# Kernel tuning notes

Measured on AMD Instinct MI355X. Metric: run time of the kernel, lower is better.

## Reference

```python
import jax, jax.numpy as jnp
import numpy as np

N_NODES = 50000
N_EDGES = 800000
D_IN = 256
DIM_H = 256
N_GRAPHS = 500
N_OUT = 10
BN_EPS = 1e-5


def _mlp(h, W1, b1, gamma, beta, mean, var, W2, b2):
    # Linear -> BatchNorm1d (eval, running stats) -> ReLU -> Linear -> ReLU
    h = h @ W1 + b1
    h = (h - mean) * (gamma / jnp.sqrt(var + BN_EPS)) + beta
    h = jax.nn.relu(h)
    return jax.nn.relu(h @ W2 + b2)


def _gin_conv(x, src, dst, params):
    # PyG GINConv with eps=0: out = nn(x + sum_{j in N(i)} x_j)
    agg = jax.ops.segment_sum(x[src], dst, num_segments=N_NODES)
    return _mlp(x + agg, *params)


def setup_inputs() -> dict:
    key = jax.random.key(0)
    ks = jax.random.split(key, 24)
    x = jax.random.normal(ks[0], (N_NODES, D_IN), dtype=jnp.float32)
    edge_index = jax.random.randint(ks[1], (2, N_EDGES), 0, N_NODES, dtype=jnp.int64)
    batch = jnp.sort(jax.random.randint(ks[2], (N_NODES,), 0, N_GRAPHS, dtype=jnp.int64))

    def lin(k, fan_in, fan_out):
        s = 1.0 / np.sqrt(fan_in)
        kw, kb = jax.random.split(k)
        W = jax.random.uniform(kw, (fan_in, fan_out), minval=-s, maxval=s, dtype=jnp.float32)
        b = jax.random.uniform(kb, (fan_out,), minval=-s, maxval=s, dtype=jnp.float32)
        return W, b

    def bn(k, d):
        k1, k2, k3, k4 = jax.random.split(k, 4)
        gamma = 1.0 + 0.1 * jax.random.normal(k1, (d,), dtype=jnp.float32)
        beta = 0.1 * jax.random.normal(k2, (d,), dtype=jnp.float32)
        mean = 0.1 * jax.random.normal(k3, (d,), dtype=jnp.float32)
        var = jax.random.uniform(k4, (d,), minval=0.5, maxval=1.5, dtype=jnp.float32)
        return gamma, beta, mean, var

    W1a, b1a = lin(ks[3], D_IN, DIM_H)
    g1a, be1a, m1a, v1a = bn(ks[4], DIM_H)
    W2a, b2a = lin(ks[5], DIM_H, DIM_H)
    W1b, b1b = lin(ks[6], DIM_H, DIM_H)
    g1b, be1b, m1b, v1b = bn(ks[7], DIM_H)
    W2b, b2b = lin(ks[8], DIM_H, DIM_H)
    lin1_W, lin1_b = lin(ks[9], DIM_H * 2, DIM_H * 3)
    lin2_W, lin2_b = lin(ks[10], DIM_H * 3, N_OUT)

    return dict(x=x, edge_index=edge_index, batch=batch,
                W1a=W1a, b1a=b1a, g1a=g1a, be1a=be1a, m1a=m1a, v1a=v1a, W2a=W2a, b2a=b2a,
                W1b=W1b, b1b=b1b, g1b=g1b, be1b=be1b, m1b=m1b, v1b=v1b, W2b=W2b, b2b=b2b,
                lin1_W=lin1_W, lin1_b=lin1_b, lin2_W=lin2_W, lin2_b=lin2_b)


def reference(x, edge_index, batch,
              W1a, b1a, g1a, be1a, m1a, v1a, W2a, b2a,
              W1b, b1b, g1b, be1b, m1b, v1b, W2b, b2b,
              lin1_W, lin1_b, lin2_W, lin2_b):
    src, dst = edge_index[0], edge_index[1]
    h1 = _gin_conv(x, src, dst, (W1a, b1a, g1a, be1a, m1a, v1a, W2a, b2a))
    h2 = _gin_conv(h1, src, dst, (W1b, b1b, g1b, be1b, m1b, v1b, W2b, b2b))
    p1 = jax.ops.segment_sum(h1, batch, num_segments=N_GRAPHS)  # global_add_pool
    p2 = jax.ops.segment_sum(h2, batch, num_segments=N_GRAPHS)
    h = jnp.concatenate([p1, p2], axis=1)
    h = jax.nn.relu(h @ lin1_W + lin1_b)
    # dropout p=0.6 is identity in eval mode
    h = h @ lin2_W + lin2_b
    return jax.nn.log_softmax(h, axis=1)
```

## Files before the change

### kernel.cpp

```cpp
#include <hip/hip_runtime.h>

#define N_NODES 50000
#define MPAD 50176
#define N_EDGES 800000
#define DIM 256
#define N_GRAPHS 500
#define N_OUT 10
#define BN_EPS 1e-5f
#define SCAN_BS 1024
#define KSPLIT 4
#define SORT_CAP 96

typedef unsigned int u32;
typedef short bf16x8 __attribute__((ext_vector_type(8)));
typedef unsigned short us8 __attribute__((ext_vector_type(8)));
typedef float f32x4 __attribute__((ext_vector_type(4)));

typedef __attribute__((address_space(1))) const unsigned int gas_u32;
typedef __attribute__((address_space(3))) unsigned int las_u32;

__device__ inline void g2l16(const void* g, void* l) {
    __builtin_amdgcn_global_load_lds((gas_u32*)g, (las_u32*)l, 16, 0, 0);
}

__device__ inline float b2f(unsigned short u) {
    union { u32 i; float f; } c; c.i = ((u32)u) << 16; return c.f;
}
__device__ inline unsigned short f2b(float f) {
    u32 x = __builtin_bit_cast(u32, f);
    return (unsigned short)((x + 0x7FFFu + ((x >> 16) & 1u)) >> 16);
}

__device__ inline int mid_addr(int row, int col) {
    return row * 512 + ((((col >> 3) ^ (row & 31)) << 4) | ((col & 7) << 1));
}

__global__ void zero_i(int* __restrict__ p, int n) {
    int i = blockIdx.x * blockDim.x + threadIdx.x;
    if (i < n) p[i] = 0;
}
__global__ void hist_dst(const int* __restrict__ dst, int* __restrict__ deg) {
    int e = blockIdx.x * blockDim.x + threadIdx.x;
    if (e < N_EDGES) atomicAdd(&deg[dst[e]], 1);
}
__global__ void scan_phase1(const int* __restrict__ deg, int* __restrict__ rowptr,
                            int* __restrict__ bsum, int n) {
    __shared__ int sh[SCAN_BS];
    int i = blockIdx.x * SCAN_BS + threadIdx.x;
    int v = (i < n) ? deg[i] : 0;
    sh[threadIdx.x] = v;
    __syncthreads();
    for (int off = 1; off < SCAN_BS; off <<= 1) {
        int t = (threadIdx.x >= off) ? sh[threadIdx.x - off] : 0;
        __syncthreads();
        sh[threadIdx.x] += t;
        __syncthreads();
    }
    if (i < n) rowptr[i] = sh[threadIdx.x] - v;
    if (threadIdx.x == SCAN_BS - 1) bsum[blockIdx.x] = sh[threadIdx.x];
}
__global__ void scan_phase2(int* __restrict__ bsum, int nb) {
    if (threadIdx.x == 0 && blockIdx.x == 0) {
        int run = 0;
        for (int b = 0; b < nb; b++) { int v = bsum[b]; bsum[b] = run; run += v; }
    }
}
__global__ void scan_phase3(int* __restrict__ rowptr, int* __restrict__ cursor,
                            const int* __restrict__ bsum, int n) {
    int i = blockIdx.x * SCAN_BS + threadIdx.x;
    if (i < n) {
        int v = rowptr[i] + bsum[blockIdx.x];
        rowptr[i] = v;
        cursor[i] = v;
    }
    if (i == 0) rowptr[n] = N_EDGES;
}
__global__ void fill_csr(const int* __restrict__ src, const int* __restrict__ dst,
                         int* __restrict__ cursor, int* __restrict__ col) {
    int e = blockIdx.x * blockDim.x + threadIdx.x;
    if (e < N_EDGES) {
        int p = atomicAdd(&cursor[dst[e]], 1);
        col[p] = src[e];
    }
}
__global__ void sort_csr(const int* __restrict__ rowptr, int* __restrict__ col) {
    __shared__ int buf[4][SORT_CAP];
    int node = blockIdx.x * 4 + (threadIdx.x >> 6);
    if (node >= N_NODES) return;
    int lane = threadIdx.x & 63;
    int w = threadIdx.x >> 6;
    int s = rowptr[node], e = rowptr[node + 1];
    int L = e - s;
    if (L <= 1 || L > SORT_CAP) return;
    for (int i = lane; i < L; i += 64) buf[w][i] = col[s + i];
    asm volatile("s_waitcnt lgkmcnt(0) vmcnt(0)" ::: "memory");
    for (int pass = 0; pass < L; pass++) {
        int base = 2 * lane + (pass & 1);
        if (base + 1 < L) {
            int a = buf[w][base], b = buf[w][base + 1];
            if (a > b) { buf[w][base] = b; buf[w][base + 1] = a; }
        }
        asm volatile("s_waitcnt lgkmcnt(0)" ::: "memory");
    }
    for (int i = lane; i < L; i += 64) col[s + i] = buf[w][i];
}
__global__ void graph_starts(const int* __restrict__ batch, int* __restrict__ gstart) {
    int g = blockIdx.x * blockDim.x + threadIdx.x;
    if (g > N_GRAPHS) return;
    if (g == N_GRAPHS) { gstart[g] = N_NODES; return; }
    int lo = 0, hi = N_NODES;
    while (lo < hi) { int mid = (lo + hi) >> 1; if (batch[mid] < g) lo = mid + 1; else hi = mid; }
    gstart[g] = lo;
}

__global__ void conv_x(const float4* __restrict__ in, ushort4* __restrict__ out, int n4) {
    int i = blockIdx.x * blockDim.x + threadIdx.x;
    if (i < n4) {
        float4 v = in[i];
        ushort4 o; o.x = f2b(v.x); o.y = f2b(v.y); o.z = f2b(v.z); o.w = f2b(v.w);
        out[i] = o;
    }
}
__global__ void conv_wt4(const float* __restrict__ W0, const float* __restrict__ W1,
                         const float* __restrict__ W2, const float* __restrict__ W3,
                         unsigned short* __restrict__ Wt) {
    int mat = blockIdx.y;
    const float* W = (mat == 0) ? W0 : (mat == 1) ? W1 : (mat == 2) ? W2 : W3;
    int n = blockIdx.x;
    int k = threadIdx.x;
    Wt[((size_t)mat << 16) + (size_t)n * 256 + k] = f2b(W[(size_t)k * 256 + n]);
}
__global__ void make_ss(const float* __restrict__ bias, const float* __restrict__ gamma,
                        const float* __restrict__ beta, const float* __restrict__ mean,
                        const float* __restrict__ var, float* __restrict__ scale,
                        float* __restrict__ shift) {
    int i = threadIdx.x;
    float s = gamma[i] * rsqrtf(var[i] + BN_EPS);
    scale[i] = s;
    shift[i] = (bias[i] - mean[i]) * s + beta[i];
}

__global__ void gather_bf(const unsigned short* __restrict__ feat,
                          const int* __restrict__ col,
                          const int* __restrict__ rowptr,
                          unsigned short* __restrict__ out) {
    int node = blockIdx.x * 4 + (threadIdx.x >> 6);
    if (node >= N_NODES) return;
    int lane = threadIdx.x & 63;
    int half = lane >> 5;
    int d8 = (lane & 31) * 8;
    float acc[8];
    #pragma unroll
    for (int j = 0; j < 8; j++) acc[j] = 0.f;
    if (half == 0) {
        us8 own = *reinterpret_cast<const us8*>(&feat[(size_t)node * DIM + d8]);
        #pragma unroll
        for (int j = 0; j < 8; j++) acc[j] = b2f((unsigned short)own[j]);
    }
    int s = rowptr[node], e = rowptr[node + 1];
    int i = s + half;
    for (; i + 6 < e; i += 8) {
        int n0 = col[i], n1 = col[i + 2], n2 = col[i + 4], n3 = col[i + 6];
        us8 v0 = *reinterpret_cast<const us8*>(&feat[(size_t)n0 * DIM + d8]);
        us8 v1 = *reinterpret_cast<const us8*>(&feat[(size_t)n1 * DIM + d8]);
        us8 v2 = *reinterpret_cast<const us8*>(&feat[(size_t)n2 * DIM + d8]);
        us8 v3 = *reinterpret_cast<const us8*>(&feat[(size_t)n3 * DIM + d8]);
        #pragma unroll
        for (int j = 0; j < 8; j++)
            acc[j] += (b2f((unsigned short)v0[j]) + b2f((unsigned short)v1[j]))
                    + (b2f((unsigned short)v2[j]) + b2f((unsigned short)v3[j]));
    }
    for (; i < e; i += 2) {
        int n0 = col[i];
        us8 v0 = *reinterpret_cast<const us8*>(&feat[(size_t)n0 * DIM + d8]);
        #pragma unroll
        for (int j = 0; j < 8; j++) acc[j] += b2f((unsigned short)v0[j]);
    }
    #pragma unroll
    for (int j = 0; j < 8; j++) acc[j] += __shfl_xor(acc[j], 32, 64);
    if (half == 0) {
        us8 o;
        #pragma unroll
        for (int j = 0; j < 8; j++) o[j] = (short)f2b(acc[j]);
        *reinterpret_cast<us8*>(&out[(size_t)node * DIM + d8]) = o;
    }
}

__global__ __launch_bounds__(256, 2)
void fused_mlp(const unsigned short* __restrict__ A,
               const unsigned short* __restrict__ W1t,
               const unsigned short* __restrict__ W2t,
               const float* __restrict__ scale1,
               const float* __restrict__ shift1,
               const float* __restrict__ shift2,
               unsigned short* __restrict__ H, int M) {
    __shared__ __align__(16) unsigned short Asb[2][64 * 32];
    __shared__ __align__(16) unsigned short Bsb[2][256 * 32];
    __shared__ __align__(16) unsigned short midb[64 * 256];

    int t = threadIdx.x;
    int wave = t >> 6, lane = t & 63;
    int m0 = blockIdx.x * 64;
    int wc = wave * 64;
    int rsel = lane & 15;
    int ksel = (lane >> 4) * 8;
    int cr = lane >> 4;

    float s1[4], sh1[4], sh2[4];
    #pragma unroll
    for (int n = 0; n < 4; n++) {
        int colg = wc + n * 16 + rsel;
        s1[n]  = scale1[colg];
        sh1[n] = shift1[colg];
        sh2[n] = shift2[colg];
    }

    int cb = (t & 3) * 16;
    const char* Ab  = (const char*)A   + (size_t)(m0 + (t >> 2)) * 512 + cb;
    const char* B1b = (const char*)W1t + (size_t)(t >> 2) * 512 + cb;
    const char* B2b = (const char*)W2t + (size_t)(t >> 2) * 512 + cb;

    f32x4 acc[4][4];
    #pragma unroll
    for (int m = 0; m < 4; m++)
        #pragma unroll
        for (int n = 0; n < 4; n++)
            acc[m][n] = (f32x4){0.f, 0.f, 0.f, 0.f};

    #pragma unroll
    for (int p = 0; p < 2; p++) {
        size_t ko = (size_t)p * 64;
        g2l16(Ab + ko, (char*)Asb[p] + (size_t)t * 16);
        #pragma unroll
        for (int i = 0; i < 4; i++)
            g2l16(B1b + (size_t)i * 32768 + ko, (char*)Bsb[p] + (size_t)(i * 256 + t) * 16);
    }

    #pragma unroll
    for (int ks = 0; ks < 8; ks++) {
        const int cur = ks & 1;
        __syncthreads();

        const unsigned short* As = Asb[cur];
        const unsigned short* Bs = Bsb[cur];
        bf16x8 af[4], bfr[4];
        #pragma unroll
        for (int m = 0; m < 4; m++)
            af[m] = *(const bf16x8*)&As[(size_t)(m * 16 + rsel) * 32 + ksel];
        #pragma unroll
        for (int n = 0; n < 4; n++)
            bfr[n] = *(const bf16x8*)&Bs[(size_t)(wc + n * 16 + rsel) * 32 + ksel];
        #pragma unroll
        for (int m = 0; m < 4; m++)
            #pragma unroll
            for (int n = 0; n < 4; n++)
                acc[m][n] = __builtin_amdgcn_mfma_f32_16x16x32_bf16(af[m], bfr[n], acc[m][n], 0, 0, 0);

        __syncthreads();
        if (ks + 2 < 8) {
            size_t ko = (size_t)(ks + 2) * 64;
            g2l16(Ab + ko, (char*)Asb[cur] + (size_t)t * 16);
            #pragma unroll
            for (int i = 0; i < 4; i++)
                g2l16(B1b + (size_t)i * 32768 + ko, (char*)Bsb[cur] + (size_t)(i * 256 + t) * 16);
        } else if (ks == 6) {
            #pragma unroll
            for (int i = 0; i < 4; i++)
                g2l16(B2b + (size_t)i * 32768, (char*)Bsb[0] + (size_t)(i * 256 + t) * 16);
        } else {
            #pragma unroll
            for (int i = 0; i < 4; i++)
                g2l16(B2b + (size_t)i * 32768 + 64, (char*)Bsb[1] + (size_t)(i * 256 + t) * 16);
        }
    }

    #pragma unroll
    for (int n = 0; n < 4; n++) {
        int colg = wc + n * 16 + rsel;
        #pragma unroll
        for (int m = 0; m < 4; m++) {
            int rowb = m * 16 + cr * 4;
            #pragma unroll
            for (int r = 0; r < 4; r++) {
                float v = fmaxf(acc[m][n][r] * s1[n] + sh1[n], 0.f);
                *(unsigned short*)((char*)midb + mid_addr(rowb + r, colg)) = f2b(v);
                acc[m][n][r] = 0.f;
            }
        }
    }

    #pragma unroll
    for (int ks = 0; ks < 8; ks++) {
        const int cur = ks & 1;
        __syncthreads();

        const unsigned short* Bs = Bsb[cur];
        bf16x8 af[4], bfr[4];
        #pragma unroll
        for (int m = 0; m < 4; m++)
            af[m] = *(const bf16x8*)((const char*)midb + mid_addr(m * 16 + rsel, ks * 32 + ksel));
        #pragma unroll
        for (int n = 0; n < 4; n++)
            bfr[n] = *(const bf16x8*)&Bs[(size_t)(wc + n * 16 + rsel) * 32 + ksel];
        #pragma unroll
        for (int m = 0; m < 4; m++)
            #pragma unroll
            for (int n = 0; n < 4; n++)
                acc[m][n] = __builtin_amdgcn_mfma_f32_16x16x32_bf16(af[m], bfr[n], acc[m][n], 0, 0, 0);

        __syncthreads();
        if (ks + 2 < 8) {
            size_t ko = (size_t)(ks + 2) * 64;
            #pragma unroll
            for (int i = 0; i < 4; i++)
                g2l16(B2b + (size_t)i * 32768 + ko, (char*)Bsb[cur] + (size_t)(i * 256 + t) * 16);
        }
    }

    #pragma unroll
    for (int n = 0; n < 4; n++) {
        int colg = wc + n * 16 + rsel;
        #pragma unroll
        for (int m = 0; m < 4; m++) {
            int rowb = m0 + m * 16 + cr * 4;
            #pragma unroll
            for (int r = 0; r < 4; r++) {
                int row = rowb + r;
                if (row < M) {
                    float v = fmaxf(acc[m][n][r] + sh2[n], 0.f);
                    H[(size_t)row * 256 + colg] = f2b(v);
                }
            }
        }
    }
}

__global__ void pool_seg(const unsigned short* __restrict__ h1,
                         const unsigned short* __restrict__ h2,
                         const int* __restrict__ gstart,
                         float* __restrict__ pcat) {
    int g = blockIdx.x;
    int t = threadIdx.x;
    int s = gstart[g], e = gstart[g + 1];
    float a1 = 0.f, a2 = 0.f;
    for (int n = s; n < e; n++) {
        a1 += b2f(h1[(size_t)n * DIM + t]);
        a2 += b2f(h2[(size_t)n * DIM + t]);
    }
    pcat[(size_t)g * 512 + t]       = a1;
    pcat[(size_t)g * 512 + 256 + t] = a2;
}

__global__ void head1(const float* __restrict__ A,
                      const float* __restrict__ W1,
                      float* __restrict__ Hpart) {
    __shared__ float As[16][65];
    __shared__ float Bs[16][65];
    int t = threadIdx.x;
    int m0 = blockIdx.y * 64;
    int n0 = blockIdx.x * 64;
    int kz = blockIdx.z * (512 / KSPLIT);
    int tx = t & 15, ty = t >> 4;
    float acc[4][4] = {};
    for (int k0 = kz; k0 < kz + 512 / KSPLIT; k0 += 16) {
        #pragma unroll
        for (int i = 0; i < 4; i++) {
            int r = (t >> 4) + i * 16;
            int k = t & 15;
            int gr = m0 + r;
            As[k][r] = (gr < N_GRAPHS) ? A[(size_t)gr * 512 + k0 + k] : 0.f;
        }
        #pragma unroll
        for (int i = 0; i < 4; i++) {
            int k = (t >> 6) + i * 4;
            int n = t & 63;
            Bs[k][n] = W1[(size_t)(k0 + k) * 768 + n0 + n];
        }
        __syncthreads();
        #pragma unroll
        for (int k = 0; k < 16; k++) {
            float a[4], b[4];
            #pragma unroll
            for (int i = 0; i < 4; i++) a[i] = As[k][ty * 4 + i];
            #pragma unroll
            for (int j = 0; j < 4; j++) b[j] = Bs[k][tx * 4 + j];
            #pragma unroll
            for (int i = 0; i < 4; i++)
                #pragma unroll
                for (int j = 0; j < 4; j++)
                    acc[i][j] += a[i] * b[j];
        }
        __syncthreads();
    }
    float* Hz = Hpart + (size_t)blockIdx.z * N_GRAPHS * 768;
    #pragma unroll
    for (int i = 0; i < 4; i++) {
        int gm = m0 + ty * 4 + i;
        if (gm >= N_GRAPHS) continue;
        #pragma unroll
        for (int j = 0; j < 4; j++) {
            int gn = n0 + tx * 4 + j;
            Hz[(size_t)gm * 768 + gn] = acc[i][j];
        }
    }
}

__global__ void head2(const float* __restrict__ Hpart, const float* __restrict__ b1,
                      const float* __restrict__ W2, const float* __restrict__ b2,
                      float* __restrict__ out) {
    int g = blockIdx.x;
    int lane = threadIdx.x;
    float part[N_OUT];
    #pragma unroll
    for (int o = 0; o < N_OUT; o++) part[o] = 0.f;
    for (int k = lane; k < 768; k += 64) {
        float hv = b1[k];
        #pragma unroll
        for (int z = 0; z < KSPLIT; z++)
            hv += Hpart[((size_t)z * N_GRAPHS + g) * 768 + k];
        hv = fmaxf(hv, 0.f);
        #pragma unroll
        for (int o = 0; o < N_OUT; o++) part[o] += hv * W2[(size_t)k * N_OUT + o];
    }
    #pragma unroll
    for (int o = 0; o < N_OUT; o++) {
        #pragma unroll
        for (int off = 32; off > 0; off >>= 1)
            part[o] += __shfl_down(part[o], off, 64);
    }
    if (lane == 0) {
        float logits[N_OUT];
        float mx = -1e30f;
        #pragma unroll
        for (int o = 0; o < N_OUT; o++) { logits[o] = part[o] + b2[o]; mx = fmaxf(mx, logits[o]); }
        float ssum = 0.f;
        #pragma unroll
        for (int o = 0; o < N_OUT; o++) ssum += expf(logits[o] - mx);
        float lse = logf(ssum);
        #pragma unroll
        for (int o = 0; o < N_OUT; o++)
            out[(size_t)g * N_OUT + o] = logits[o] - mx - lse;
    }
}

extern "C" void kernel_launch(void* const* d_in, const int* in_sizes, int n_in,
                              void* d_out, int out_size, void* d_ws, size_t ws_size,
                              hipStream_t stream) {
    const float* x     = (const float*)d_in[0];
    const int*   ei    = (const int*)d_in[1];
    const int*   batch = (const int*)d_in[2];
    const float* W1a = (const float*)d_in[3];
    const float* b1a = (const float*)d_in[4];
    const float* g1a = (const float*)d_in[5];
    const float* be1a= (const float*)d_in[6];
    const float* m1a = (const float*)d_in[7];
    const float* v1a = (const float*)d_in[8];
    const float* W2a = (const float*)d_in[9];
    const float* b2a = (const float*)d_in[10];
    const float* W1b = (const float*)d_in[11];
    const float* b1b = (const float*)d_in[12];
    const float* g1b = (const float*)d_in[13];
    const float* be1b= (const float*)d_in[14];
    const float* m1b = (const float*)d_in[15];
    const float* v1b = (const float*)d_in[16];
    const float* W2b = (const float*)d_in[17];
    const float* b2b = (const float*)d_in[18];
    const float* lin1_W = (const float*)d_in[19];
    const float* lin1_b = (const float*)d_in[20];
    const float* lin2_W = (const float*)d_in[21];
    const float* lin2_b = (const float*)d_in[22];

    const size_t NBUF = (size_t)MPAD * DIM;
    char* ws = (char*)d_ws;
    unsigned short* agg  = (unsigned short*)ws;            ws += NBUF * 2;
    unsigned short* h1   = (unsigned short*)ws;            ws += NBUF * 2;
    unsigned short* h2   = (unsigned short*)ws;            ws += NBUF * 2;
    unsigned short* x_bf = (unsigned short*)ws;            ws += (size_t)N_NODES * DIM * 2;
    unsigned short* Wt   = (unsigned short*)ws;            ws += 4 * 65536 * 2;
    float* ss    = (float*)ws;                             ws += 4 * 256 * 4;
    float* pcat  = (float*)ws;                             ws += (size_t)N_GRAPHS * 512 * 4;
    float* Hpart = (float*)ws;                             ws += (size_t)KSPLIT * N_GRAPHS * 768 * 4;
    int* deg     = (int*)ws;                               ws += (size_t)N_NODES * 4;
    int* cursor  = (int*)ws;                               ws += (size_t)N_NODES * 4;
    int* rowptr  = (int*)ws;                               ws += (size_t)(N_NODES + 1) * 4;
    int* bsum    = (int*)ws;                               ws += 64 * 4;
    int* col     = (int*)ws;                               ws += (size_t)N_EDGES * 4;
    int* gstart  = (int*)ws;

    const int* srcE = ei;
    const int* dstE = ei + N_EDGES;

    const int nscan = (N_NODES + SCAN_BS - 1) / SCAN_BS;

    zero_i<<<(N_NODES + 255) / 256, 256, 0, stream>>>(deg, N_NODES);
    hist_dst<<<(N_EDGES + 255) / 256, 256, 0, stream>>>(dstE, deg);
    scan_phase1<<<nscan, SCAN_BS, 0, stream>>>(deg, rowptr, bsum, N_NODES);
    scan_phase2<<<1, 64, 0, stream>>>(bsum, nscan);
    scan_phase3<<<nscan, SCAN_BS, 0, stream>>>(rowptr, cursor, bsum, N_NODES);
    fill_csr<<<(N_EDGES + 255) / 256, 256, 0, stream>>>(srcE, dstE, cursor, col);
    sort_csr<<<(N_NODES + 3) / 4, 256, 0, stream>>>(rowptr, col);
    graph_starts<<<2, 256, 0, stream>>>(batch, gstart);

    conv_x<<<(N_NODES * DIM / 4 + 255) / 256, 256, 0, stream>>>(
        (const float4*)x, (ushort4*)x_bf, N_NODES * DIM / 4);
    dim3 wt_grid(256, 4);
    conv_wt4<<<wt_grid, 256, 0, stream>>>(W1a, W2a, W1b, W2b, Wt);
    make_ss<<<1, 256, 0, stream>>>(b1a, g1a, be1a, m1a, v1a, ss + 0 * 512, ss + 0 * 512 + 256);
    make_ss<<<1, 256, 0, stream>>>(b1b, g1b, be1b, m1b, v1b, ss + 1 * 512, ss + 1 * 512 + 256);

    gather_bf<<<(N_NODES + 3) / 4, 256, 0, stream>>>(x_bf, col, rowptr, agg);
    fused_mlp<<<MPAD / 64, 256, 0, stream>>>(agg, Wt + 0 * 65536, Wt + 1 * 65536,
                                             ss + 0 * 512, ss + 0 * 512 + 256, b2a, h1, N_NODES);

    gather_bf<<<(N_NODES + 3) / 4, 256, 0, stream>>>(h1, col, rowptr, agg);
    fused_mlp<<<MPAD / 64, 256, 0, stream>>>(agg, Wt + 2 * 65536, Wt + 3 * 65536,
                                             ss + 1 * 512, ss + 1 * 512 + 256, b2b, h2, N_NODES);

    pool_seg<<<N_GRAPHS, 256, 0, stream>>>(h1, h2, gstart, pcat);
    dim3 h1grid(12, 8, KSPLIT);
    head1<<<h1grid, 256, 0, stream>>>(pcat, lin1_W, Hpart);
    head2<<<N_GRAPHS, 64, 0, stream>>>(Hpart, lin1_b, lin2_W, lin2_b, (float*)d_out);
}
```

Measured before the change: 396.6 us.

## Split neighbor gather into feature-slice passes with 16 edge lanes per wave

The gather kernel now launches 8 passes over the grid, each covering a 32-column slice of the feature dimension. Within a wave, 16 lane groups handle different edges and 4 lanes cover the 32 columns, and the partial sums are combined with a butterfly shuffle. The aim is more edges in flight per node and a smaller per-pass working set that may stay in cache across neighbors. In exchange, the col indices are re-read 8 times, each row fetch is only a 64-byte segment, and the reduction needs more shuffles.

```diff
diff --git a/kernel.cpp b/kernel.cpp
--- a/kernel.cpp
+++ b/kernel.cpp
@@ -140,49 +140,41 @@
     shift[i] = (bias[i] - mean[i]) * s + beta[i];
 }
 
-__global__ void gather_bf(const unsigned short* __restrict__ feat,
+__global__ void gather_ps(const unsigned short* __restrict__ feat,
                           const int* __restrict__ col,
                           const int* __restrict__ rowptr,
                           unsigned short* __restrict__ out) {
     int node = blockIdx.x * 4 + (threadIdx.x >> 6);
     if (node >= N_NODES) return;
+    int pass = blockIdx.y;
     int lane = threadIdx.x & 63;
-    int half = lane >> 5;
-    int d8 = (lane & 31) * 8;
+    int eg = lane >> 2;
+    int dbase = pass * 32 + (lane & 3) * 8;
+
     float acc[8];
     #pragma unroll
     for (int j = 0; j < 8; j++) acc[j] = 0.f;
-    if (half == 0) {
-        us8 own = *reinterpret_cast<const us8*>(&feat[(size_t)node * DIM + d8]);
+    if (eg == 0) {
+        us8 own = *reinterpret_cast<const us8*>(&feat[(size_t)node * DIM + dbase]);
         #pragma unroll
         for (int j = 0; j < 8; j++) acc[j] = b2f((unsigned short)own[j]);
     }
     int s = rowptr[node], e = rowptr[node + 1];
-    int i = s + half;
-    for (; i + 6 < e; i += 8) {
-        int n0 = col[i], n1 = col[i + 2], n2 = col[i + 4], n3 = col[i + 6];
-        us8 v0 = *reinterpret_cast<const us8*>(&feat[(size_t)n0 * DIM + d8]);
-        us8 v1 = *reinterpret_cast<const us8*>(&feat[(size_t)n1 * DIM + d8]);
-        us8 v2 = *reinterpret_cast<const us8*>(&feat[(size_t)n2 * DIM + d8]);
-        us8 v3 = *reinterpret_cast<const us8*>(&feat[(size_t)n3 * DIM + d8]);
-        #pragma unroll
-        for (int j = 0; j < 8; j++)
-            acc[j] += (b2f((unsigned short)v0[j]) + b2f((unsigned short)v1[j]))
-                    + (b2f((unsigned short)v2[j]) + b2f((unsigned short)v3[j]));
-    }
-    for (; i < e; i += 2) {
-        int n0 = col[i];
-        us8 v0 = *reinterpret_cast<const us8*>(&feat[(size_t)n0 * DIM + d8]);
-        #pragma unroll
-        for (int j = 0; j < 8; j++) acc[j] += b2f((unsigned short)v0[j]);
-    }
-    #pragma unroll
-    for (int j = 0; j < 8; j++) acc[j] += __shfl_xor(acc[j], 32, 64);
-    if (half == 0) {
+    for (int i = s + eg; i < e; i += 16) {
+        int src = col[i];
+        us8 v = *reinterpret_cast<const us8*>(&feat[(size_t)src * DIM + dbase]);
+        #pragma unroll
+        for (int j = 0; j < 8; j++) acc[j] += b2f((unsigned short)v[j]);
+    }
+    #pragma unroll
+    for (int m = 4; m <= 32; m <<= 1)
+        #pragma unroll
+        for (int j = 0; j < 8; j++) acc[j] += __shfl_xor(acc[j], m, 64);
+    if (eg == 0) {
         us8 o;
         #pragma unroll
         for (int j = 0; j < 8; j++) o[j] = (short)f2b(acc[j]);
-        *reinterpret_cast<us8*>(&out[(size_t)node * DIM + d8]) = o;
+        *reinterpret_cast<us8*>(&out[(size_t)node * DIM + dbase]) = o;
     }
 }
 
@@ -508,11 +500,13 @@
     make_ss<<<1, 256, 0, stream>>>(b1a, g1a, be1a, m1a, v1a, ss + 0 * 512, ss + 0 * 512 + 256);
     make_ss<<<1, 256, 0, stream>>>(b1b, g1b, be1b, m1b, v1b, ss + 1 * 512, ss + 1 * 512 + 256);
 
-    gather_bf<<<(N_NODES + 3) / 4, 256, 0, stream>>>(x_bf, col, rowptr, agg);
+    dim3 ggrid((N_NODES + 3) / 4, 8);
+
+    gather_ps<<<ggrid, 256, 0, stream>>>(x_bf, col, rowptr, agg);
     fused_mlp<<<MPAD / 64, 256, 0, stream>>>(agg, Wt + 0 * 65536, Wt + 1 * 65536,
                                              ss + 0 * 512, ss + 0 * 512 + 256, b2a, h1, N_NODES);
 
-    gather_bf<<<(N_NODES + 3) / 4, 256, 0, stream>>>(h1, col, rowptr, agg);
+    gather_ps<<<ggrid, 256, 0, stream>>>(h1, col, rowptr, agg);
     fused_mlp<<<MPAD / 64, 256, 0, stream>>>(agg, Wt + 2 * 65536, Wt + 3 * 65536,
                                              ss + 1 * 512, ss + 1 * 512 + 256, b2b, h2, N_NODES);
 
```

Result: slower. 568.4 us (+43.3%).
